# Optimization experiments

Hardware: AMD Instinct MI355X
Metric: run time of the kernel (lower is better)

## Reference

```python
import jax, jax.numpy as jnp
import numpy as np

DIM, DEPTH, HEADS, DIM_HEAD, MLP = 768, 6, 12, 64, 3072
INNER = HEADS * DIM_HEAD
B, N = 8, 1024
SCALE = DIM_HEAD ** -0.5
EPS = 1e-5


def _ln(x, g, b):
    m = jnp.mean(x, -1, keepdims=True)
    v = jnp.mean(jnp.square(x - m), -1, keepdims=True)
    return (x - m) * jax.lax.rsqrt(v + EPS) * g + b


def _ternary(w):
    # BitNet-style ternary quant with straight-through estimator
    s = jnp.mean(jnp.abs(w)) + 1e-8
    wq = jnp.clip(jnp.round(w / s), -1.0, 1.0) * s
    return w + jax.lax.stop_gradient(wq - w)


def setup_inputs() -> dict:
    key = jax.random.key(0)
    ks = jax.random.split(key, 8)
    d = {
        'x': jax.random.normal(ks[0], (B, N, DIM), jnp.float32),
        'ln1_g': jnp.ones((DEPTH, DIM), jnp.float32),
        'ln1_b': jnp.zeros((DEPTH, DIM), jnp.float32),
        'Wqkv': jax.random.normal(ks[1], (DEPTH, 3 * INNER, DIM), jnp.float32) * 0.02,
        'ln2_g': jnp.ones((DEPTH, INNER), jnp.float32),
        'ln2_b': jnp.zeros((DEPTH, INNER), jnp.float32),
        'Wo': jax.random.normal(ks[2], (DEPTH, DIM, INNER), jnp.float32) * 0.02,
        'bo': jnp.zeros((DEPTH, DIM), jnp.float32),
        'ffln1_g': jnp.ones((DEPTH, DIM), jnp.float32),
        'ffln1_b': jnp.zeros((DEPTH, DIM), jnp.float32),
        'W1': jax.random.normal(ks[3], (DEPTH, MLP, DIM), jnp.float32) * 0.02,
        'b1': jnp.zeros((DEPTH, MLP), jnp.float32),
        'ffln2_g': jnp.ones((DEPTH, MLP), jnp.float32),
        'ffln2_b': jnp.zeros((DEPTH, MLP), jnp.float32),
        'W2': jax.random.normal(ks[4], (DEPTH, DIM, MLP), jnp.float32) * 0.02,
        'b2': jnp.zeros((DEPTH, DIM), jnp.float32),
    }
    return d


def _forward(x, ln1_g, ln1_b, Wqkv, ln2_g, ln2_b, Wo, bo,
             ffln1_g, ffln1_b, W1, b1, ffln2_g, ffln2_b, W2, b2):
    depth = Wqkv.shape[0]
    # layers 0..depth-2 ternary, last layer plain linear
    flag = jnp.concatenate([jnp.ones((depth - 1,), x.dtype), jnp.zeros((1,), x.dtype)])

    def block(h, p):
        (g1, b1n, wqkv, g2, b2n, wo, bo_, fg1, fb1, w1, bb1, fg2, fb2, w2, bb2, f) = p

        def mt(w):
            return f * _ternary(w) + (1.0 - f) * w

        y = _ln(h, g1, b1n)
        qkv = jnp.einsum('bnd,ed->bne', y, mt(wqkv))  # [B,N,3*INNER]
        q, k, v = jnp.split(qkv, 3, axis=-1)
        def heads(t):
            return t.reshape(B, N, HEADS, DIM_HEAD).transpose(0, 2, 1, 3)
        q, k, v = heads(q), heads(k), heads(v)
        attn = jax.nn.softmax(jnp.einsum('bhnd,bhmd->bhnm', q, k) * SCALE, axis=-1)
        o = jnp.einsum('bhnm,bhmd->bhnd', attn, v)
        o = o.transpose(0, 2, 1, 3).reshape(B, N, INNER)
        o = _ln(o, g2, b2n)
        o = jnp.einsum('bne,de->bnd', o, mt(wo)) + bo_
        h = h + o
        y = _ln(h, fg1, fb1)
        y = jnp.einsum('bnd,md->bnm', y, mt(w1)) + bb1
        y = jax.nn.gelu(y, approximate=False)
        y = _ln(y, fg2, fb2)
        y = jnp.einsum('bnm,dm->bnd', y, mt(w2)) + bb2
        return h + y, None

    xs = (ln1_g, ln1_b, Wqkv, ln2_g, ln2_b, Wo, bo,
          ffln1_g, ffln1_b, W1, b1, ffln2_g, ffln2_b, W2, b2, flag)
    out, _ = jax.lax.scan(block, x, xs)
    return out


def reference(x, ln1_g, ln1_b, Wqkv, ln2_g, ln2_b, Wo, bo,
              ffln1_g, ffln1_b, W1, b1, ffln2_g, ffln2_b, W2, b2):
    return _forward(x, ln1_g, ln1_b, Wqkv, ln2_g, ln2_b, Wo, bo,
                    ffln1_g, ffln1_b, W1, b1, ffln2_g, ffln2_b, W2, b2)
```

## Files before the change

### kernel.cpp

```cpp
#include <hip/hip_runtime.h>
#include <hip/hip_bf16.h>
#include <math.h>

typedef __bf16 bf16_t;
typedef __bf16 bf16x4 __attribute__((ext_vector_type(4)));
typedef __bf16 bf16x8 __attribute__((ext_vector_type(8)));
typedef float  f32x4  __attribute__((ext_vector_type(4)));

#define TOKENS 8192
#define DIMV   768
#define INNERV 768
#define QKVW   2304
#define MLPW   3072
#define NSEQ   1024
#define NB     8
#define NH     12
#define DH     64

enum { EP_STORE = 0, EP_BIAS_RES = 1, EP_BIAS_GELU = 2 };

__device__ __forceinline__ void gload_lds16(const bf16_t* g, bf16_t* l)
{
  __builtin_amdgcn_global_load_lds((const __attribute__((address_space(1))) void*)g,
                                   (__attribute__((address_space(3))) void*)l,
                                   16, 0, 0);
}

__device__ __forceinline__ float gelu_fast(float x)
{
  const float z = fabsf(x) * 0.70710678118654752f;
  const float d = fmaf(0.3275911f, z, 1.0f);
  const float t = 1.0f / d;
  float p = fmaf(t, 1.061405429f, -1.453152027f);
  p = fmaf(t, p, 1.421413741f);
  p = fmaf(t, p, -0.284496736f);
  p = fmaf(t, p, 0.254829592f);
  p = t * p;
  const float e = __expf(-z * z);
  float erfv = fmaf(-p, e, 1.0f);
  erfv = copysignf(erfv, x);
  return 0.5f * x * (1.0f + erfv);
}

template <int BM>
__global__ __launch_bounds__(256)
void gemm_nt(const bf16_t* __restrict__ A, const bf16_t* __restrict__ B,
             const int K, const int N, const int mode,
             const float* __restrict__ sacc_p, const float sinvn, const float sbias,
             const float* __restrict__ bias,
             float* __restrict__ resid,
             bf16_t* __restrict__ outb,
             float* __restrict__ fout)
{
  constexpr int MI = BM / 32;
  constexpr int WR = BM / 2;
  __shared__ __align__(16) bf16_t lsAll[3 * BM * 32 + 3 * 128 * 32];
  bf16_t* lsA = lsAll;
  bf16_t* lsB = lsAll + 3 * BM * 32;
  const int tid  = threadIdx.x;
  const int lane = tid & 63;
  const int wave = tid >> 6;
  const int wm = wave >> 1, wn = wave & 1;
  const int bm = blockIdx.x, bn = blockIdx.y;

  const int srB   = wave * 32 + (lane >> 2);
  const int fswB  = (srB >> 1) & 3;
  const int scolB = ((lane & 3) ^ fswB) * 8;
  const bf16_t* gB = B + (size_t)(bn * 128 + srB) * K + scolB;
  const int lb0 = srB * 32 + (lane & 3) * 8;
  const int lb1 = (srB + 16) * 32 + (lane & 3) * 8;

  const int srA   = (BM == 128) ? srB : (wave * 16 + (lane >> 2));
  const int fswA  = (srA >> 1) & 3;
  const int scolA = ((lane & 3) ^ fswA) * 8;
  const bf16_t* gA = A + (size_t)(bm * BM + srA) * K + scolA;
  const int la0 = srA * 32 + (lane & 3) * 8;
  const int la1 = (srA + 16) * 32 + (lane & 3) * 8;

  f32x4 acc[MI][4];
#pragma unroll
  for (int i = 0; i < MI; i++)
#pragma unroll
    for (int j = 0; j < 4; j++) acc[i][j] = (f32x4){0.f, 0.f, 0.f, 0.f};

  const int fr   = ((lane & 15) >> 1) & 3;
  const int rsl  = ((lane >> 4) ^ fr) * 8;
  const int arow = (wm * WR + (lane & 15)) * 32 + rsl;
  const int brow = (wn * 64 + (lane & 15)) * 32 + rsl;

  auto stage = [&](int b, int kb) {
    gload_lds16(gA + kb, &lsA[b * BM * 32 + la0]);
    if constexpr (BM == 128) gload_lds16(gA + (size_t)16 * K + kb, &lsA[b * BM * 32 + la1]);
    gload_lds16(gB + kb, &lsB[b * 128 * 32 + lb0]);
    gload_lds16(gB + (size_t)16 * K + kb, &lsB[b * 128 * 32 + lb1]);
  };
  auto compute = [&](int b) {
    bf16x8 af[MI], bfv[4];
#pragma unroll
    for (int i = 0; i < MI; i++) af[i]  = *(const bf16x8*)&lsA[b * BM * 32 + arow + i * 16 * 32];
#pragma unroll
    for (int j = 0; j < 4; j++)  bfv[j] = *(const bf16x8*)&lsB[b * 128 * 32 + brow + j * 16 * 32];
#pragma unroll
    for (int i = 0; i < MI; i++)
#pragma unroll
      for (int j = 0; j < 4; j++)
        acc[i][j] = __builtin_amdgcn_mfma_f32_16x16x32_bf16(af[i], bfv[j], acc[i][j], 0, 0, 0);
  };

  const int NT = K / 32;
  stage(0, 0);
  stage(1, 32);
  int cb = 0, sb = 2;
  for (int t = 0; t < NT - 1; ++t) {
    if constexpr (BM == 128) asm volatile("s_waitcnt vmcnt(4)" ::: "memory");
    else                     asm volatile("s_waitcnt vmcnt(3)" ::: "memory");
    __builtin_amdgcn_s_barrier();
    __builtin_amdgcn_sched_barrier(0);
    compute(cb);
    if (t + 2 < NT) stage(sb, (t + 2) * 32);
    cb = (cb == 2) ? 0 : cb + 1;
    sb = (sb == 2) ? 0 : sb + 1;
  }
  asm volatile("s_waitcnt vmcnt(0)" ::: "memory");
  __builtin_amdgcn_s_barrier();
  __builtin_amdgcn_sched_barrier(0);
  compute(cb);

  __syncthreads();
  const float s = (*sacc_p) * sinvn + sbias;
  const int lr0 = wm * WR + (lane >> 4) * 4;
  const int lc0 = wn * 64 + (lane & 15);

  if (mode == EP_BIAS_RES) {
    float* ep = (float*)lsAll;
#pragma unroll
    for (int i = 0; i < MI; i++)
#pragma unroll
      for (int j = 0; j < 4; j++) {
        const float bcol = bias[bn * 128 + lc0 + j * 16];
#pragma unroll
        for (int r = 0; r < 4; r++)
          ep[(lr0 + i * 16 + r) * 132 + lc0 + j * 16] = acc[i][j][r] * s + bcol;
      }
    __syncthreads();
#pragma unroll
    for (int it = 0; it < BM / 8; ++it) {
      const int lr = it * 8 + (tid >> 5);
      const int lc = (tid & 31) * 4;
      f32x4 v = *(const f32x4*)&ep[lr * 132 + lc];
      const size_t idx = (size_t)(bm * BM + lr) * N + bn * 128 + lc;
      f32x4 rv = *(const f32x4*)&resid[idx];
      if (fout) *(f32x4*)&fout[idx]  = rv + v;
      else      *(f32x4*)&resid[idx] = rv + v;
    }
  } else {
    bf16_t* ep = lsAll;
#pragma unroll
    for (int i = 0; i < MI; i++)
#pragma unroll
      for (int j = 0; j < 4; j++) {
        const int col = bn * 128 + lc0 + j * 16;
#pragma unroll
        for (int r = 0; r < 4; r++) {
          const float v = acc[i][j][r] * s;
          ep[(lr0 + i * 16 + r) * 136 + lc0 + j * 16] =
              (mode == EP_STORE) ? (bf16_t)v : (bf16_t)gelu_fast(v + bias[col]);
        }
      }
    __syncthreads();
#pragma unroll
    for (int it = 0; it < BM / 16; ++it) {
      const int lr = it * 16 + (tid >> 4);
      const int lc = (tid & 15) * 8;
      bf16x8 v = *(const bf16x8*)&ep[lr * 136 + lc];
      *(bf16x8*)&outb[(size_t)(bm * BM + lr) * N + bn * 128 + lc] = v;
    }
  }
}

template <typename TIN>
__global__ __launch_bounds__(256)
void ln_kern(const TIN* __restrict__ x, const float* __restrict__ g,
             const float* __restrict__ b, bf16_t* __restrict__ y, const int W)
{
  const int row = blockIdx.x;
  const int tid = threadIdx.x;
  const TIN* xr = x + (size_t)row * W;
  float s = 0.f, s2 = 0.f;
  if constexpr (sizeof(TIN) == 4) {
    const f32x4* xv = (const f32x4*)xr;
    for (int i = tid; i < W / 4; i += 256) {
      f32x4 v = xv[i];
#pragma unroll
      for (int e = 0; e < 4; e++) { s += v[e]; s2 += v[e] * v[e]; }
    }
  } else {
    const bf16x8* xv = (const bf16x8*)xr;
    for (int i = tid; i < W / 8; i += 256) {
      bf16x8 v = xv[i];
#pragma unroll
      for (int e = 0; e < 8; e++) { const float f = (float)v[e]; s += f; s2 += f * f; }
    }
  }
#pragma unroll
  for (int off = 32; off > 0; off >>= 1) {
    s  += __shfl_xor(s,  off, 64);
    s2 += __shfl_xor(s2, off, 64);
  }
  __shared__ float red[8];
  if ((tid & 63) == 0) { red[(tid >> 6) * 2] = s; red[(tid >> 6) * 2 + 1] = s2; }
  __syncthreads();
  const float ts  = red[0] + red[2] + red[4] + red[6];
  const float ts2 = red[1] + red[3] + red[5] + red[7];
  const float invW = 1.0f / (float)W;
  const float mean = ts * invW;
  const float var  = fmaxf(ts2 * invW - mean * mean, 0.f);
  const float rs   = rsqrtf(var + 1e-5f);
  bf16_t* yr = y + (size_t)row * W;
  const f32x4* gv = (const f32x4*)g;
  const f32x4* bv = (const f32x4*)b;
  if constexpr (sizeof(TIN) == 4) {
    const f32x4* xv = (const f32x4*)xr;
    bf16x4* yv = (bf16x4*)yr;
    for (int i = tid; i < W / 4; i += 256) {
      f32x4 v = xv[i], gg = gv[i], bb = bv[i];
      bf16x4 o;
#pragma unroll
      for (int e = 0; e < 4; e++) o[e] = (bf16_t)((v[e] - mean) * rs * gg[e] + bb[e]);
      yv[i] = o;
    }
  } else {
    const bf16x8* xv = (const bf16x8*)xr;
    bf16x8* yv = (bf16x8*)yr;
    for (int i = tid; i < W / 8; i += 256) {
      bf16x8 v = xv[i];
      f32x4 g0 = gv[2 * i], g1 = gv[2 * i + 1];
      f32x4 b0 = bv[2 * i], b1 = bv[2 * i + 1];
      bf16x8 o;
#pragma unroll
      for (int e = 0; e < 4; e++) o[e]     = (bf16_t)(((float)v[e]     - mean) * rs * g0[e] + b0[e]);
#pragma unroll
      for (int e = 0; e < 4; e++) o[e + 4] = (bf16_t)(((float)v[e + 4] - mean) * rs * g1[e] + b1[e]);
      yv[i] = o;
    }
  }
}

__global__ __launch_bounds__(512)
void attn_mfma(const bf16_t* __restrict__ qkv, bf16_t* __restrict__ o)
{
  __shared__ __align__(16) bf16_t Ks[64][72];
  __shared__ __align__(16) bf16_t Vt[64][72];
  __shared__ __align__(16) bf16_t Pw[8][16][72];
  const float SCL = 0.125f * 1.44269504088896f;
  const int tid  = threadIdx.x;
  const int lane = tid & 63;
  const int wave = tid >> 6;
  const int quad = lane >> 4;
  const int l15  = lane & 15;

  const int id      = blockIdx.x;
  const int logical = (id & 7) * 96 + (id >> 3);
  const int qb   = logical & 7;
  const int rest = logical >> 3;
  const int hh   = rest % 12;
  const int bb   = rest / 12;
  const size_t tokbase = (size_t)bb * NSEQ;

  const int qrow = qb * 128 + wave * 16 + l15;
  bf16x8 qf[2];
  {
    const bf16_t* qp = qkv + (tokbase + qrow) * QKVW + hh * DH;
    qf[0] = *(const bf16x8*)(qp + quad * 8);
    qf[1] = *(const bf16x8*)(qp + 32 + quad * 8);
  }

  f32x4 Ot[4];
#pragma unroll
  for (int i = 0; i < 4; i++) Ot[i] = (f32x4){0.f, 0.f, 0.f, 0.f};
  float m2[4], lp[4];
#pragma unroll
  for (int r = 0; r < 4; r++) { m2[r] = -1e30f; lp[r] = 0.f; }

  const int srow = tid & 63;
  const int sd   = (tid >> 6) * 8;

  bf16x8 k0, v0;
  {
    const bf16_t* kp = qkv + (tokbase + srow) * QKVW + INNERV + hh * DH + sd;
    k0 = *(const bf16x8*)kp;
    v0 = *(const bf16x8*)(kp + INNERV);
  }

  for (int kt = 0; kt < NSEQ / 64; ++kt) {
    __syncthreads();
    *(bf16x8*)&Ks[srow][sd] = k0;
#pragma unroll
    for (int e = 0; e < 8; e++) Vt[sd + e][srow] = v0[e];
    __syncthreads();

    bf16x8 nk0 = k0, nv0 = v0;
    if (kt + 1 < NSEQ / 64) {
      const bf16_t* kp = qkv + (tokbase + (kt + 1) * 64 + srow) * QKVW + INNERV + hh * DH + sd;
      nk0 = *(const bf16x8*)kp;
      nv0 = *(const bf16x8*)(kp + INNERV);
    }

    f32x4 st[4];
    __builtin_amdgcn_s_setprio(1);
#pragma unroll
    for (int nt = 0; nt < 4; nt++) {
      bf16x8 b0 = *(const bf16x8*)&Ks[nt * 16 + l15][quad * 8];
      bf16x8 b1 = *(const bf16x8*)&Ks[nt * 16 + l15][32 + quad * 8];
      f32x4 c = (f32x4){0.f, 0.f, 0.f, 0.f};
      c = __builtin_amdgcn_mfma_f32_16x16x32_bf16(qf[0], b0, c, 0, 0, 0);
      c = __builtin_amdgcn_mfma_f32_16x16x32_bf16(qf[1], b1, c, 0, 0, 0);
      st[nt] = c;
    }
    __builtin_amdgcn_s_setprio(0);

    float lm[4];
#pragma unroll
    for (int r = 0; r < 4; r++)
      lm[r] = fmaxf(fmaxf(st[0][r], st[1][r]), fmaxf(st[2][r], st[3][r]));
    const bool ok = (lm[0] * SCL <= m2[0] + 8.f) && (lm[1] * SCL <= m2[1] + 8.f) &&
                    (lm[2] * SCL <= m2[2] + 8.f) && (lm[3] * SCL <= m2[3] + 8.f);
    if (!__all(ok)) {
#pragma unroll
      for (int r = 0; r < 4; r++) {
        float v = lm[r];
        v = fmaxf(v, __shfl_xor(v, 1, 64));
        v = fmaxf(v, __shfl_xor(v, 2, 64));
        v = fmaxf(v, __shfl_xor(v, 4, 64));
        v = fmaxf(v, __shfl_xor(v, 8, 64));
        const float rmax2 = v * SCL;
        const float mnew = fmaxf(m2[r], rmax2);
        const float alpha = exp2f(m2[r] - mnew);
        m2[r] = mnew;
        lp[r] *= alpha;
#pragma unroll
        for (int dt = 0; dt < 4; dt++) Ot[dt][r] *= alpha;
      }
    }
#pragma unroll
    for (int nt = 0; nt < 4; nt++) {
#pragma unroll
      for (int r = 0; r < 4; r++) {
        const float p = exp2f(fmaf(st[nt][r], SCL, -m2[r]));
        lp[r] += p;
        Pw[wave][quad * 4 + r][nt * 16 + l15] = (bf16_t)p;
      }
    }

    asm volatile("s_waitcnt lgkmcnt(0)" ::: "memory");
    __builtin_amdgcn_sched_barrier(0);

    __builtin_amdgcn_s_setprio(1);
#pragma unroll
    for (int kk = 0; kk < 2; kk++) {
      bf16x8 pa = *(const bf16x8*)&Pw[wave][l15][kk * 32 + quad * 8];
#pragma unroll
      for (int dt = 0; dt < 4; dt++) {
        bf16x8 vb = *(const bf16x8*)&Vt[dt * 16 + l15][kk * 32 + quad * 8];
        Ot[dt] = __builtin_amdgcn_mfma_f32_16x16x32_bf16(pa, vb, Ot[dt], 0, 0, 0);
      }
    }
    __builtin_amdgcn_s_setprio(0);

    k0 = nk0; v0 = nv0;
  }

  float inv[4];
#pragma unroll
  for (int r = 0; r < 4; r++) {
    float v = lp[r];
    v += __shfl_xor(v, 1, 64);
    v += __shfl_xor(v, 2, 64);
    v += __shfl_xor(v, 4, 64);
    v += __shfl_xor(v, 8, 64);
    inv[r] = 1.0f / v;
  }
#pragma unroll
  for (int dt = 0; dt < 4; dt++) {
#pragma unroll
    for (int r = 0; r < 4; r++) {
      const int q = qb * 128 + wave * 16 + quad * 4 + r;
      const int d = dt * 16 + l15;
      o[(tokbase + q) * INNERV + hh * DH + d] = (bf16_t)(Ot[dt][r] * inv[r]);
    }
  }
}

__global__ __launch_bounds__(64)
void zero_kern(float* __restrict__ p)
{
  p[threadIdx.x] = 0.f;
}

__global__ __launch_bounds__(256)
void absmean4_kern(const float* __restrict__ w0, const float* __restrict__ w1,
                   const float* __restrict__ w2, const float* __restrict__ w3,
                   const long n0, const long n1, const long n2, const long n3,
                   float* __restrict__ acc)
{
  const int t = blockIdx.y;
  const float* w = (t == 0) ? w0 : (t == 1) ? w1 : (t == 2) ? w2 : w3;
  const long  n  = (t == 0) ? n0 : (t == 1) ? n1 : (t == 2) ? n2 : n3;
  const int tid = threadIdx.x;
  float s = 0.f;
  const size_t stride = (size_t)256 * gridDim.x * 4;
  for (size_t i = ((size_t)blockIdx.x * 256 + tid) * 4; i < (size_t)n; i += stride) {
    f32x4 v = *(const f32x4*)(w + i);
    s += fabsf(v[0]) + fabsf(v[1]) + fabsf(v[2]) + fabsf(v[3]);
  }
#pragma unroll
  for (int off = 32; off > 0; off >>= 1) s += __shfl_xor(s, off, 64);
  __shared__ float red[4];
  if ((tid & 63) == 0) red[tid >> 6] = s;
  __syncthreads();
  if (tid == 0) atomicAdd(&acc[t], red[0] + red[1] + red[2] + red[3]);
}

__global__ __launch_bounds__(256)
void quant4_kern(const float* __restrict__ w0, const float* __restrict__ w1,
                 const float* __restrict__ w2, const float* __restrict__ w3,
                 bf16_t* __restrict__ q0, bf16_t* __restrict__ q1,
                 bf16_t* __restrict__ q2, bf16_t* __restrict__ q3,
                 const int n40, const int n41, const int n42, const int n43,
                 const float* __restrict__ acc,
                 const float inv0, const float inv1, const float inv2, const float inv3)
{
  const int t = blockIdx.y;
  const float* w = (t == 0) ? w0 : (t == 1) ? w1 : (t == 2) ? w2 : w3;
  bf16_t*      q = (t == 0) ? q0 : (t == 1) ? q1 : (t == 2) ? q2 : q3;
  const int   n4 = (t == 0) ? n40 : (t == 1) ? n41 : (t == 2) ? n42 : n43;
  const float iv = (t == 0) ? inv0 : (t == 1) ? inv1 : (t == 2) ? inv2 : inv3;
  const int i = blockIdx.x * 256 + threadIdx.x;
  if (i >= n4) return;
  const float s = acc[t] * iv + 1e-8f;
  f32x4 v = ((const f32x4*)w)[i];
  bf16x4 o;
#pragma unroll
  for (int e = 0; e < 4; e++) {
    float qv = rintf(v[e] / s);
    qv = fminf(1.f, fmaxf(-1.f, qv));
    o[e] = (bf16_t)qv;
  }
  ((bf16x4*)q)[i] = o;
}

__global__ __launch_bounds__(256)
void cast4_kern(const float* __restrict__ w0, const float* __restrict__ w1,
                const float* __restrict__ w2, const float* __restrict__ w3,
                bf16_t* __restrict__ q0, bf16_t* __restrict__ q1,
                bf16_t* __restrict__ q2, bf16_t* __restrict__ q3,
                const int n40, const int n41, const int n42, const int n43)
{
  const int t = blockIdx.y;
  const float* w = (t == 0) ? w0 : (t == 1) ? w1 : (t == 2) ? w2 : w3;
  bf16_t*      q = (t == 0) ? q0 : (t == 1) ? q1 : (t == 2) ? q2 : q3;
  const int   n4 = (t == 0) ? n40 : (t == 1) ? n41 : (t == 2) ? n42 : n43;
  const int i = blockIdx.x * 256 + threadIdx.x;
  if (i >= n4) return;
  f32x4 v = ((const f32x4*)w)[i];
  bf16x4 o;
#pragma unroll
  for (int e = 0; e < 4; e++) o[e] = (bf16_t)v[e];
  ((bf16x4*)q)[i] = o;
}

__global__ __launch_bounds__(256)
void copyf_kern(const float* __restrict__ in, float* __restrict__ out, const int n4)
{
  const int i = blockIdx.x * 256 + threadIdx.x;
  if (i < n4) ((f32x4*)out)[i] = ((const f32x4*)in)[i];
}

extern "C" void kernel_launch(void* const* d_in, const int* in_sizes, int n_in,
                              void* d_out, int out_size, void* d_ws, size_t ws_size,
                              hipStream_t stream)
{
  const float* x     = (const float*)d_in[0];
  const float* ln1_g = (const float*)d_in[1];
  const float* ln1_b = (const float*)d_in[2];
  const float* Wqkv  = (const float*)d_in[3];
  const float* ln2_g = (const float*)d_in[4];
  const float* ln2_b = (const float*)d_in[5];
  const float* Wo    = (const float*)d_in[6];
  const float* bo    = (const float*)d_in[7];
  const float* fg1   = (const float*)d_in[8];
  const float* fb1   = (const float*)d_in[9];
  const float* W1    = (const float*)d_in[10];
  const float* b1    = (const float*)d_in[11];
  const float* fg2   = (const float*)d_in[12];
  const float* fb2   = (const float*)d_in[13];
  const float* W2    = (const float*)d_in[14];
  const float* b2    = (const float*)d_in[15];

  char* ws = (char*)d_ws;
  size_t off = 0;
  float*  sacc  = (float*)(ws + off);  off += 256;
  float*  h     = (float*)(ws + off);  off += (size_t)TOKENS * DIMV * 4;
  bf16_t* bigA  = (bf16_t*)(ws + off); off += (size_t)TOKENS * MLPW * 2;
  bf16_t* bigB  = (bf16_t*)(ws + off); off += (size_t)TOKENS * MLPW * 2;
  bf16_t* q_qkv = (bf16_t*)(ws + off); off += (size_t)QKVW * DIMV * 2;
  bf16_t* q_o   = (bf16_t*)(ws + off); off += (size_t)DIMV * INNERV * 2;
  bf16_t* q_1   = (bf16_t*)(ws + off); off += (size_t)MLPW * DIMV * 2;
  bf16_t* q_2   = (bf16_t*)(ws + off); off += (size_t)DIMV * MLPW * 2;

  bf16_t* obuf   = bigA;
  bf16_t* ln2out = bigA + (size_t)TOKENS * INNERV;

  zero_kern<<<1, 64, 0, stream>>>(sacc);
  copyf_kern<<<TOKENS * DIMV / 4 / 256, 256, 0, stream>>>(x, h, TOKENS * DIMV / 4);

  for (int lyr = 0; lyr < 6; ++lyr) {
    const float* wqkv_l = Wqkv + (size_t)lyr * QKVW * DIMV;
    const float* wo_l   = Wo   + (size_t)lyr * DIMV * INNERV;
    const float* w1_l   = W1   + (size_t)lyr * MLPW * DIMV;
    const float* w2_l   = W2   + (size_t)lyr * DIMV * MLPW;
    const float *sq, *so, *s1, *s2p;
    float iq, io, i1, i2, bq, bo2, bb1v, bb2v;
    if (lyr < 5) {
      absmean4_kern<<<dim3(256, 4), 256, 0, stream>>>(
          wqkv_l, wo_l, w1_l, w2_l,
          (long)QKVW * DIMV, (long)DIMV * INNERV, (long)MLPW * DIMV, (long)DIMV * MLPW,
          &sacc[lyr * 4]);
      quant4_kern<<<dim3(MLPW * DIMV / 1024, 4), 256, 0, stream>>>(
          wqkv_l, wo_l, w1_l, w2_l, q_qkv, q_o, q_1, q_2,
          QKVW * DIMV / 4, DIMV * INNERV / 4, MLPW * DIMV / 4, DIMV * MLPW / 4,
          &sacc[lyr * 4],
          1.0f / (QKVW * DIMV), 1.0f / (DIMV * INNERV), 1.0f / (MLPW * DIMV), 1.0f / (DIMV * MLPW));
      sq = &sacc[lyr * 4 + 0]; iq = 1.0f / (QKVW * DIMV); bq = 1e-8f;
      so = &sacc[lyr * 4 + 1]; io = 1.0f / (DIMV * INNERV); bo2 = 1e-8f;
      s1 = &sacc[lyr * 4 + 2]; i1 = 1.0f / (MLPW * DIMV); bb1v = 1e-8f;
      s2p = &sacc[lyr * 4 + 3]; i2 = 1.0f / (DIMV * MLPW); bb2v = 1e-8f;
    } else {
      cast4_kern<<<dim3(MLPW * DIMV / 1024, 4), 256, 0, stream>>>(
          wqkv_l, wo_l, w1_l, w2_l, q_qkv, q_o, q_1, q_2,
          QKVW * DIMV / 4, DIMV * INNERV / 4, MLPW * DIMV / 4, DIMV * MLPW / 4);
      sq = so = s1 = s2p = &sacc[63];
      iq = io = i1 = i2 = 0.f;
      bq = bo2 = bb1v = bb2v = 1.0f;
    }

    ln_kern<float><<<TOKENS, 256, 0, stream>>>(h, ln1_g + lyr * DIMV, ln1_b + lyr * DIMV, bigA, DIMV);
    gemm_nt<128><<<dim3(64, QKVW / 128), 256, 0, stream>>>(bigA, q_qkv, DIMV, QKVW, EP_STORE, sq, iq, bq, nullptr, nullptr, bigB, nullptr);
    attn_mfma<<<NSEQ / 128 * NH * NB, 512, 0, stream>>>(bigB, obuf);
    ln_kern<bf16_t><<<TOKENS, 256, 0, stream>>>(obuf, ln2_g + lyr * INNERV, ln2_b + lyr * INNERV, ln2out, INNERV);
    gemm_nt<64><<<dim3(TOKENS / 64, DIMV / 128), 256, 0, stream>>>(ln2out, q_o, INNERV, DIMV, EP_BIAS_RES, so, io, bo2, bo + lyr * DIMV, h, nullptr, nullptr);
    ln_kern<float><<<TOKENS, 256, 0, stream>>>(h, fg1 + lyr * DIMV, fb1 + lyr * DIMV, bigA, DIMV);
    gemm_nt<128><<<dim3(64, MLPW / 128), 256, 0, stream>>>(bigA, q_1, DIMV, MLPW, EP_BIAS_GELU, s1, i1, bb1v, b1 + lyr * MLPW, nullptr, bigB, nullptr);
    ln_kern<bf16_t><<<TOKENS, 256, 0, stream>>>(bigB, fg2 + lyr * MLPW, fb2 + lyr * MLPW, bigA, MLPW);
    gemm_nt<64><<<dim3(TOKENS / 64, DIMV / 128), 256, 0, stream>>>(bigA, q_2, MLPW, DIMV, EP_BIAS_RES, s2p, i2, bb2v, b2 + lyr * DIMV, h, nullptr,
                                                                   (lyr == 5) ? (float*)d_out : nullptr);
  }
}
```

Baseline: 2.126 ms.

## Add 256x128-tile GEMM kernel for QKV and FFN-up projections

Adds a new GEMM kernel with a 256x128 output tile per block, where each wave computes a 128x64 sub-tile. It uses double-buffered direct global-to-LDS loads with explicit waitcnt and barrier scheduling. The epilogue stages bf16 results through LDS so global stores are coalesced. The QKV and W1 projections switch to it, which reduces redundant operand loads per FLOP. In exchange it holds more accumulator registers (128 floats per thread), which lowers occupancy, and it launches fewer blocks, which may leave CUs less evenly loaded.

```diff
diff --git a/kernel.cpp b/kernel.cpp
--- a/kernel.cpp
+++ b/kernel.cpp
@@ -40,6 +40,124 @@
   float erfv = fmaf(-p, e, 1.0f);
   erfv = copysignf(erfv, x);
   return 0.5f * x * (1.0f + erfv);
+}
+
+__global__ __launch_bounds__(256)
+void gemm_big(const bf16_t* __restrict__ A, const bf16_t* __restrict__ B,
+              const int K, const int N, const int mode,
+              const float* __restrict__ sacc_p, const float sinvn, const float sbias,
+              const float* __restrict__ bias,
+              bf16_t* __restrict__ outb)
+{
+  __shared__ __align__(16) bf16_t lsAll[2 * 256 * 32 + 2 * 128 * 32];
+  bf16_t* lsA = lsAll;
+  bf16_t* lsB = lsAll + 2 * 256 * 32;
+  const int tid  = threadIdx.x;
+  const int lane = tid & 63;
+  const int wave = tid >> 6;
+  const int wm = wave >> 1, wn = wave & 1;
+  const int bm = blockIdx.x, bn = blockIdx.y;
+
+  const int srA   = wave * 64 + (lane >> 2);
+  const int fswA  = (srA >> 1) & 3;
+  const int scolA = ((lane & 3) ^ fswA) * 8;
+  const bf16_t* gA = A + (size_t)(bm * 256 + srA) * K + scolA;
+  const int laa = srA * 32 + (lane & 3) * 8;
+  const int srB   = wave * 32 + (lane >> 2);
+  const int fswB  = (srB >> 1) & 3;
+  const int scolB = ((lane & 3) ^ fswB) * 8;
+  const bf16_t* gB = B + (size_t)(bn * 128 + srB) * K + scolB;
+  const int lbb = srB * 32 + (lane & 3) * 8;
+
+  f32x4 acc[8][4];
+#pragma unroll
+  for (int i = 0; i < 8; i++)
+#pragma unroll
+    for (int j = 0; j < 4; j++) acc[i][j] = (f32x4){0.f, 0.f, 0.f, 0.f};
+
+  const int fr   = ((lane & 15) >> 1) & 3;
+  const int rsl  = ((lane >> 4) ^ fr) * 8;
+  const int arow = (wm * 128 + (lane & 15)) * 32 + rsl;
+  const int brow = (wn * 64 + (lane & 15)) * 32 + rsl;
+
+  auto stage = [&](int b, int kb) {
+    bf16_t* la = lsA + b * 256 * 32;
+    bf16_t* lb = lsB + b * 128 * 32;
+    gload_lds16(gA + kb,                  &la[laa]);
+    gload_lds16(gA + (size_t)16 * K + kb, &la[laa + 16 * 32]);
+    gload_lds16(gA + (size_t)32 * K + kb, &la[laa + 32 * 32]);
+    gload_lds16(gA + (size_t)48 * K + kb, &la[laa + 48 * 32]);
+    gload_lds16(gB + kb,                  &lb[lbb]);
+    gload_lds16(gB + (size_t)16 * K + kb, &lb[lbb + 16 * 32]);
+  };
+  auto compute = [&](int b) {
+    const bf16_t* la = lsA + b * 256 * 32;
+    const bf16_t* lb = lsB + b * 128 * 32;
+    bf16x8 bfv[4];
+#pragma unroll
+    for (int j = 0; j < 4; j++) bfv[j] = *(const bf16x8*)&lb[brow + j * 16 * 32];
+#pragma unroll
+    for (int i = 0; i < 8; i++) {
+      bf16x8 af = *(const bf16x8*)&la[arow + i * 16 * 32];
+#pragma unroll
+      for (int j = 0; j < 4; j++)
+        acc[i][j] = __builtin_amdgcn_mfma_f32_16x16x32_bf16(af, bfv[j], acc[i][j], 0, 0, 0);
+    }
+  };
+
+  const int NT = K / 32;
+  stage(0, 0);
+  stage(1, 32);
+  int cur = 0;
+  for (int t = 0; t < NT - 1; ++t) {
+    asm volatile("s_waitcnt vmcnt(6)" ::: "memory");
+    __builtin_amdgcn_s_barrier();
+    __builtin_amdgcn_sched_barrier(0);
+    compute(cur);
+    asm volatile("s_waitcnt lgkmcnt(0)" ::: "memory");
+    __builtin_amdgcn_s_barrier();
+    __builtin_amdgcn_sched_barrier(0);
+    if (t + 2 < NT) stage(cur, (t + 2) * 32);
+    cur ^= 1;
+  }
+  asm volatile("s_waitcnt vmcnt(0)" ::: "memory");
+  __builtin_amdgcn_s_barrier();
+  __builtin_amdgcn_sched_barrier(0);
+  compute(cur);
+
+  __syncthreads();
+  const float s = (*sacc_p) * sinvn + sbias;
+  const int quad = lane >> 4;
+  const int l15  = lane & 15;
+  bf16_t* ep = lsAll;
+#pragma unroll
+  for (int h = 0; h < 2; ++h) {
+    if (wm == h) {
+#pragma unroll
+      for (int i = 0; i < 8; i++)
+#pragma unroll
+        for (int j = 0; j < 4; j++) {
+          const int lc  = wn * 64 + l15 + j * 16;
+          const int col = bn * 128 + lc;
+#pragma unroll
+          for (int r = 0; r < 4; r++) {
+            const int lr = i * 16 + quad * 4 + r;
+            const float v = acc[i][j][r] * s;
+            ep[lr * 136 + lc] =
+                (mode == EP_STORE) ? (bf16_t)v : (bf16_t)gelu_fast(v + bias[col]);
+          }
+        }
+    }
+    __syncthreads();
+#pragma unroll
+    for (int it = 0; it < 8; ++it) {
+      const int lr = it * 16 + (tid >> 4);
+      const int lc = (tid & 15) * 8;
+      bf16x8 v = *(const bf16x8*)&ep[lr * 136 + lc];
+      *(bf16x8*)&outb[(size_t)(bm * 256 + h * 128 + lr) * N + bn * 128 + lc] = v;
+    }
+    __syncthreads();
+  }
 }
 
 template <int BM>
@@ -545,12 +663,12 @@
     }
 
     ln_kern<float><<<TOKENS, 256, 0, stream>>>(h, ln1_g + lyr * DIMV, ln1_b + lyr * DIMV, bigA, DIMV);
-    gemm_nt<128><<<dim3(64, QKVW / 128), 256, 0, stream>>>(bigA, q_qkv, DIMV, QKVW, EP_STORE, sq, iq, bq, nullptr, nullptr, bigB, nullptr);
+    gemm_big<<<dim3(TOKENS / 256, QKVW / 128), 256, 0, stream>>>(bigA, q_qkv, DIMV, QKVW, EP_STORE, sq, iq, bq, nullptr, bigB);
     attn_mfma<<<NSEQ / 128 * NH * NB, 512, 0, stream>>>(bigB, obuf);
     ln_kern<bf16_t><<<TOKENS, 256, 0, stream>>>(obuf, ln2_g + lyr * INNERV, ln2_b + lyr * INNERV, ln2out, INNERV);
     gemm_nt<64><<<dim3(TOKENS / 64, DIMV / 128), 256, 0, stream>>>(ln2out, q_o, INNERV, DIMV, EP_BIAS_RES, so, io, bo2, bo + lyr * DIMV, h, nullptr, nullptr);
     ln_kern<float><<<TOKENS, 256, 0, stream>>>(h, fg1 + lyr * DIMV, fb1 + lyr * DIMV, bigA, DIMV);
-    gemm_nt<128><<<dim3(64, MLPW / 128), 256, 0, stream>>>(bigA, q_1, DIMV, MLPW, EP_BIAS_GELU, s1, i1, bb1v, b1 + lyr * MLPW, nullptr, bigB, nullptr);
+    gemm_big<<<dim3(TOKENS / 256, MLPW / 128), 256, 0, stream>>>(bigA, q_1, DIMV, MLPW, EP_BIAS_GELU, s1, i1, bb1v, b1 + lyr * MLPW, bigB);
     ln_kern<bf16_t><<<TOKENS, 256, 0, stream>>>(bigB, fg2 + lyr * MLPW, fb2 + lyr * MLPW, bigA, MLPW);
     gemm_nt<64><<<dim3(TOKENS / 64, DIMV / 128), 256, 0, stream>>>(bigA, q_2, MLPW, DIMV, EP_BIAS_RES, s2p, i2, bb2v, b2 + lyr * DIMV, h, nullptr,
                                                                    (lyr == 5) ? (float*)d_out : nullptr);
```

Result: slower. 3.015 ms (+41.8%).
